# Kernel optimization log

Hardware: AMD Instinct MI355X
Metric: run time of the kernel (lower is better)

The kernel has to match this reference:

```python
import jax, jax.numpy as jnp
import numpy as np

B, S, N_USERS, N_ITEMS, E = 32, 512, 10000, 10000, 128


def setup_inputs() -> dict:
    key = jax.random.key(0)
    ks = jax.random.split(key, 8)
    users = jax.random.randint(ks[0], (B, S), 0, N_USERS, dtype=jnp.int32)
    items = jax.random.randint(ks[1], (B, S), 0, N_ITEMS, dtype=jnp.int32)
    user_mem0 = jax.random.normal(ks[2], (B, N_USERS, E), dtype=jnp.float32)
    item_mem0 = jax.random.normal(ks[3], (B, N_ITEMS, E), dtype=jnp.float32)
    # GRUCell(2E, E): w_ih (3E, 2E), w_hh (3E, E)
    w_ih = jax.random.normal(ks[4], (3 * E, 2 * E), dtype=jnp.float32) * 0.05
    w_hh = jax.random.normal(ks[5], (3 * E, E), dtype=jnp.float32) * 0.05
    b_ih = jax.random.normal(ks[6], (3 * E,), dtype=jnp.float32) * 0.05
    b_hh = jax.random.normal(ks[7], (3 * E,), dtype=jnp.float32) * 0.05
    return {"users": users, "items": items, "user_mem0": user_mem0,
            "item_mem0": item_mem0, "w_ih": w_ih, "w_hh": w_hh,
            "b_ih": b_ih, "b_hh": b_hh}


def _gru_cell(x, h, w_ih, w_hh, b_ih, b_hh):
    # torch.nn.GRUCell semantics
    gi = x @ w_ih.T + b_ih  # (B, 3E)
    gh = h @ w_hh.T + b_hh  # (B, 3E)
    i_r, i_z, i_n = jnp.split(gi, 3, axis=-1)
    h_r, h_z, h_n = jnp.split(gh, 3, axis=-1)
    r = jax.nn.sigmoid(i_r + h_r)
    z = jax.nn.sigmoid(i_z + h_z)
    n = jnp.tanh(i_n + r * h_n)
    return (1.0 - z) * n + z * h


def reference(users, items, user_mem0, item_mem0, w_ih, w_hh, b_ih, b_hh):
    batch = jnp.arange(users.shape[0])

    def step(carry, uv):
        um, im = carry
        u, it = uv  # (B,), (B,)
        ue = um[batch, u]   # gather (B, E)
        ie = im[batch, it]  # gather (B, E)
        xu = jnp.concatenate([ue, ie], axis=-1)
        xi = jnp.concatenate([ie, ue], axis=-1)
        nu = _gru_cell(xu, ue, w_ih, w_hh, b_ih, b_hh)
        ni = _gru_cell(xi, ie, w_ih, w_hh, b_ih, b_hh)
        um = um.at[batch, u].set(nu)   # scatter write
        im = im.at[batch, it].set(ni)  # scatter write
        return (um, im), (nu, ni)

    (_, _), (u_out, i_out) = jax.lax.scan(
        step, (user_mem0, item_mem0), (users.T, items.T))
    # (S, B, E) -> (B, S, E)
    return jnp.transpose(u_out, (1, 0, 2)), jnp.transpose(i_out, (1, 0, 2))
```

## Files before the change

### kernel.cpp

```cpp
#include <hip/hip_runtime.h>

#define NB 32
#define NS 512
#define NE 128
#define NU 10000

#define WS_PREVU 0
#define WS_PREVI 16384
#define WS_RCNT  32768
#define WS_LCNT  32864
#define WS_GL    32896
#define WS_LATE  82048
#define WS_WBF   98432

typedef __attribute__((ext_vector_type(8))) short bf16x8;
typedef __attribute__((ext_vector_type(4))) float f32x4;

__device__ __forceinline__ unsigned short f2bf(float f) {
    unsigned int u = __float_as_uint(f);
    u += 0x7fff + ((u >> 16) & 1);
    return (unsigned short)(u >> 16);
}

#define BARRIER() do { \
    asm volatile("s_waitcnt lgkmcnt(0)" ::: "memory"); \
    __builtin_amdgcn_s_barrier(); \
    __builtin_amdgcn_sched_barrier(0); \
} while (0)

__global__ __launch_bounds__(512) void prep_kernel(
    const int* __restrict__ users, const int* __restrict__ items,
    const float* __restrict__ w_ih, const float* __restrict__ w_hh, int* ws)
{
    const int blk = blockIdx.x, tid = threadIdx.x;
    if (blk >= 32) {
        const int base = (blk - 32) * 4096 + tid * 8;
        const int r = base >> 7, k = base & 127;
        const float* src;
        if (r < 384)      src = w_ih + (size_t)r * 256 + k;
        else if (r < 768) src = w_ih + (size_t)(r - 384) * 256 + 128 + k;
        else              src = w_hh + (size_t)(r - 768) * 128 + k;
        unsigned short* wbf = (unsigned short*)(ws + WS_WBF);
#pragma unroll
        for (int j = 0; j < 8; ++j) wbf[base + j] = f2bf(src[j]);
        return;
    }
    const int b = blk;
    __shared__ int s_u[NS], s_i[NS];
    __shared__ unsigned char s_r[NS];
    __shared__ int cnt[3], s_chg;
    s_u[tid] = users[b * NS + tid];
    s_i[tid] = items[b * NS + tid];
    if (tid < 3) cnt[tid] = 0;
    __syncthreads();
    const int mu = s_u[tid], mi = s_i[tid];
    int pu = -1, pi = -1;
    for (int u = tid - 1; u >= 0 && ((pu < 0) | (pi < 0)); u -= 8) {
        int vu[8], vi[8];
#pragma unroll
        for (int j = 0; j < 8; ++j) {
            const int uu = u - j;
            vu[j] = (uu >= 0) ? s_u[uu] : -1;
            vi[j] = (uu >= 0) ? s_i[uu] : -1;
        }
#pragma unroll
        for (int j = 0; j < 8; ++j) {
            if (pu < 0 && vu[j] == mu) pu = u - j;
            if (pi < 0 && vi[j] == mi) pi = u - j;
        }
    }
    ws[WS_PREVU + (b << 9) + tid] = pu;
    ws[WS_PREVI + (b << 9) + tid] = pi;
    s_r[tid] = (pu < 0 && pi < 0) ? 0 : 255;
    __syncthreads();
    for (int pass = 0; pass < 16; ++pass) {
        if (tid == 0) s_chg = 0;
        __syncthreads();
        if (s_r[tid] == 255) {
            const int ru = pu < 0 ? -1 : (int)s_r[pu];
            const int ri = pi < 0 ? -1 : (int)s_r[pi];
            if (ru != 255 && ri != 255) {
                int rr = 1 + (ru > ri ? ru : ri);
                if (rr > 3) rr = 3;
                s_r[tid] = (unsigned char)rr;
                s_chg = 1;
            }
        }
        __syncthreads();
        if (!s_chg) break;
    }
    const int r = s_r[tid];
    if (r < 3) {
        const int slot = atomicAdd(&cnt[r], 1);
        ws[WS_GL + (r * 32 + b) * 512 + slot] = tid;
    }
    __syncthreads();
    if (tid < 3) ws[WS_RCNT + tid * 32 + b] = cnt[tid];
    if (tid == 0) {
        int n = 0;
        for (int t = 0; t < NS; ++t)
            if (s_r[t] >= 3) { ws[WS_LATE + (b << 9) + n] = t; ++n; }
        ws[WS_LCNT + b] = n;
    }
}

__global__ __launch_bounds__(512, 1) void rg_kernel(
    const int* __restrict__ users, const int* __restrict__ items,
    const float* __restrict__ umem0, const float* __restrict__ imem0,
    const float* __restrict__ b_ih, const float* __restrict__ b_hh,
    const int* __restrict__ ws, float* uout, float* iout, int r)
{
    const int b = blockIdx.x & 31, sblk = blockIdx.x >> 5;
    const int cnt = ws[WS_RCNT + r * 32 + b];
    const int nch = (cnt + 7) >> 3;
    if (sblk >= nch) return;
    const int tid = threadIdx.x;
    const int lane = tid & 63, wave = tid >> 6;
    const int col = lane & 15, kgrp = lane >> 4;

    __shared__ __align__(16) float yl[16 * 1156];
    __shared__ __align__(16) float xf[16 * 132];
    __shared__ __align__(16) unsigned short xb[16 * 136];
    __shared__ float b6[768];
    __shared__ unsigned long long srcs[2][16];
    __shared__ unsigned long long hdst[2][16];

    for (int i = tid; i < 768; i += 512)
        b6[i] = i < 384 ? b_ih[i] : b_hh[i - 384];

    const unsigned short* wbf = (const unsigned short*)(ws + WS_WBF);
    bf16x8 wfrag[9][4];
#pragma unroll
    for (int m9 = 0; m9 < 9; ++m9) {
        const int row = wave * 144 + m9 * 16 + col;
#pragma unroll
        for (int kt = 0; kt < 4; ++kt)
            wfrag[m9][kt] = *(const bf16x8*)&wbf[row * 128 + kt * 32 + kgrp * 8];
    }

    const int* glist = ws + WS_GL + (r * 32 + b) * 512;
    const int* prevU = ws + WS_PREVU + (b << 9);
    const int* prevI = ws + WS_PREVI + (b << 9);

#define META(LC, SEL) do { \
    if (tid < 16) { \
        const int j = (LC) * 8 + (tid >> 1); \
        unsigned long long sp = 0, hd = 0; \
        if (j < cnt) { \
            const int t = glist[j]; \
            const int node = (b << 9) + t; \
            const int cell = tid & 1; \
            const int p = cell ? prevI[t] : prevU[t]; \
            const float* s; \
            if (p < 0) { \
                const int ix = cell ? items[node] : users[node]; \
                s = (cell ? imem0 : umem0) + ((size_t)b * NU + ix) * NE; \
            } else { \
                s = (cell ? iout : uout) + ((size_t)((b << 9) + p)) * NE; \
            } \
            sp = (unsigned long long)s; \
            hd = (unsigned long long)((cell ? iout : uout) + (size_t)node * NE); \
        } \
        srcs[SEL][tid] = sp; hdst[SEL][tid] = hd; \
    } \
} while (0)

    const int gc = tid >> 5, ge4 = (tid & 31) * 4;
    int cur = 0;
    META(sblk, 0);
    BARRIER();
    float4 v = (float4){0.f, 0.f, 0.f, 0.f};
    {
        const float* s = (const float*)srcs[0][gc];
        if (s) v = *(const float4*)(s + ge4);
    }

    for (int lc = sblk; lc < nch; lc += 8) {
        const int nxt = cur ^ 1;
        const bool hasnext = (lc + 8) < nch;
        if (hasnext) META(lc + 8, nxt);
        if (hdst[cur][gc]) {
            *(float4*)&xf[gc * 132 + ge4] = v;
            ushort4 w4;
            w4.x = f2bf(v.x); w4.y = f2bf(v.y);
            w4.z = f2bf(v.z); w4.w = f2bf(v.w);
            *(ushort4*)&xb[gc * 136 + ge4] = w4;
        }
        BARRIER();
        float4 vn = (float4){0.f, 0.f, 0.f, 0.f};
        if (hasnext) {
            const float* s = (const float*)srcs[nxt][gc];
            if (s) vn = *(const float4*)(s + ge4);
        }
        {
            bf16x8 bfrag[4];
#pragma unroll
            for (int kt = 0; kt < 4; ++kt)
                bfrag[kt] = *(const bf16x8*)&xb[col * 136 + kt * 32 + kgrp * 8];
            f32x4 acc[9];
#pragma unroll
            for (int m9 = 0; m9 < 9; ++m9) acc[m9] = (f32x4){0.f, 0.f, 0.f, 0.f};
#pragma unroll
            for (int kt = 0; kt < 4; ++kt)
#pragma unroll
                for (int m9 = 0; m9 < 9; ++m9)
                    acc[m9] = __builtin_amdgcn_mfma_f32_16x16x32_bf16(
                        wfrag[m9][kt], bfrag[kt], acc[m9], 0, 0, 0);
#pragma unroll
            for (int m9 = 0; m9 < 9; ++m9)
                *(f32x4*)&yl[col * 1156 + wave * 144 + m9 * 16 + kgrp * 4] = acc[m9];
        }
        BARRIER();
#pragma unroll
        for (int it = 0; it < 4; ++it) {
            const int idx = tid + it * 512;
            const int c = idx >> 7, e = idx & 127;
            float* hb = (float*)hdst[cur][c];
            if (hb) {
                const float* ys = &yl[c * 1156];
                const float* yo = &yl[(c ^ 1) * 1156];
                const float gir = ys[e]        + yo[384 + e] + b6[e];
                const float giz = ys[128 + e]  + yo[512 + e] + b6[128 + e];
                const float gin = ys[256 + e]  + yo[640 + e] + b6[256 + e];
                const float ghr = ys[768 + e]  + b6[384 + e];
                const float ghz = ys[896 + e]  + b6[512 + e];
                const float ghn = ys[1024 + e] + b6[640 + e];
                const float rr = 1.f / (1.f + __expf(-(gir + ghr)));
                const float z  = 1.f / (1.f + __expf(-(giz + ghz)));
                const float pre = gin + rr * ghn;
                const float nn = 2.f / (1.f + __expf(-2.f * pre)) - 1.f;
                hb[e] = (1.f - z) * nn + z * xf[c * 132 + e];
            }
        }
        BARRIER();
        v = vn; cur = nxt;
    }
#undef META
}

__global__ __launch_bounds__(512, 1) void cleanup_kernel(
    const int* __restrict__ users, const int* __restrict__ items,
    const float* __restrict__ umem0, const float* __restrict__ imem0,
    const float* __restrict__ b_ih, const float* __restrict__ b_hh,
    const int* __restrict__ ws, float* uout, float* iout)
{
    const int b = blockIdx.x;
    const int cnt2 = ws[WS_RCNT + 64 + b];
    const int cntL = ws[WS_LCNT + b];
    if (cnt2 + cntL == 0) return;
    const int tid = threadIdx.x;
    const int lane = tid & 63, wave = tid >> 6;
    const int col = lane & 15, kgrp = lane >> 4;

    __shared__ __align__(16) float yl[16 * 1156];
    __shared__ __align__(16) float xf[16 * 132];
    __shared__ __align__(16) unsigned short xb[16 * 136];
    __shared__ float b6[768];
    __shared__ unsigned long long srcs[16];
    __shared__ unsigned long long hdst[16];

    for (int i = tid; i < 768; i += 512)
        b6[i] = i < 384 ? b_ih[i] : b_hh[i - 384];

    const unsigned short* wbf = (const unsigned short*)(ws + WS_WBF);
    bf16x8 wfrag[9][4];
#pragma unroll
    for (int m9 = 0; m9 < 9; ++m9) {
        const int row = wave * 144 + m9 * 16 + col;
#pragma unroll
        for (int kt = 0; kt < 4; ++kt)
            wfrag[m9][kt] = *(const bf16x8*)&wbf[row * 128 + kt * 32 + kgrp * 8];
    }

    const int* prevU = ws + WS_PREVU + (b << 9);
    const int* prevI = ws + WS_PREVI + (b << 9);

    for (int ph = 0; ph < 2; ++ph) {
        const int cntn = ph == 0 ? cnt2 : cntL;
        const int base = ph == 0 ? WS_GL + (64 + b) * 512 : WS_LATE + (b << 9);
        const int step = ph == 0 ? 8 : 1;
        for (int j0 = 0; j0 < cntn; j0 += step) {
            const int n = (cntn - j0 < step) ? (cntn - j0) : step;
            if (tid < 16) {
                const int jj = tid >> 1;
                unsigned long long sp = 0, hd = 0;
                if (jj < n) {
                    const int t = ws[base + j0 + jj];
                    const int node = (b << 9) + t;
                    const int cell = tid & 1;
                    const int p = cell ? prevI[t] : prevU[t];
                    const float* s;
                    if (p < 0) {
                        const int ix = cell ? items[node] : users[node];
                        s = (cell ? imem0 : umem0) + ((size_t)b * NU + ix) * NE;
                    } else {
                        s = (cell ? iout : uout) + ((size_t)((b << 9) + p)) * NE;
                    }
                    sp = (unsigned long long)s;
                    hd = (unsigned long long)((cell ? iout : uout) + (size_t)node * NE);
                }
                srcs[tid] = sp; hdst[tid] = hd;
            }
            __syncthreads();
            {
                const int c = tid >> 5, e4 = (tid & 31) * 4;
                const float* s = (const float*)srcs[c];
                if (s) {
                    const float4 vv = *(const float4*)(s + e4);
                    *(float4*)&xf[c * 132 + e4] = vv;
                    ushort4 w4;
                    w4.x = f2bf(vv.x); w4.y = f2bf(vv.y);
                    w4.z = f2bf(vv.z); w4.w = f2bf(vv.w);
                    *(ushort4*)&xb[c * 136 + e4] = w4;
                }
            }
            __syncthreads();
            {
                bf16x8 bfrag[4];
#pragma unroll
                for (int kt = 0; kt < 4; ++kt)
                    bfrag[kt] = *(const bf16x8*)&xb[col * 136 + kt * 32 + kgrp * 8];
                f32x4 acc[9];
#pragma unroll
                for (int m9 = 0; m9 < 9; ++m9) acc[m9] = (f32x4){0.f, 0.f, 0.f, 0.f};
#pragma unroll
                for (int kt = 0; kt < 4; ++kt)
#pragma unroll
                    for (int m9 = 0; m9 < 9; ++m9)
                        acc[m9] = __builtin_amdgcn_mfma_f32_16x16x32_bf16(
                            wfrag[m9][kt], bfrag[kt], acc[m9], 0, 0, 0);
#pragma unroll
                for (int m9 = 0; m9 < 9; ++m9)
                    *(f32x4*)&yl[col * 1156 + wave * 144 + m9 * 16 + kgrp * 4] = acc[m9];
            }
            __syncthreads();
#pragma unroll
            for (int it = 0; it < 4; ++it) {
                const int idx = tid + it * 512;
                const int c = idx >> 7, e = idx & 127;
                float* hb = (float*)hdst[c];
                if (hb) {
                    const float* ys = &yl[c * 1156];
                    const float* yo = &yl[(c ^ 1) * 1156];
                    const float gir = ys[e]        + yo[384 + e] + b6[e];
                    const float giz = ys[128 + e]  + yo[512 + e] + b6[128 + e];
                    const float gin = ys[256 + e]  + yo[640 + e] + b6[256 + e];
                    const float ghr = ys[768 + e]  + b6[384 + e];
                    const float ghz = ys[896 + e]  + b6[512 + e];
                    const float ghn = ys[1024 + e] + b6[640 + e];
                    const float rr = 1.f / (1.f + __expf(-(gir + ghr)));
                    const float z  = 1.f / (1.f + __expf(-(giz + ghz)));
                    const float pre = gin + rr * ghn;
                    const float nn = 2.f / (1.f + __expf(-2.f * pre)) - 1.f;
                    hb[e] = (1.f - z) * nn + z * xf[c * 132 + e];
                }
            }
            __threadfence();
            __syncthreads();
        }
    }
}

extern "C" void kernel_launch(void* const* d_in, const int* in_sizes, int n_in,
                              void* d_out, int out_size, void* d_ws, size_t ws_size,
                              hipStream_t stream) {
    const int*   users = (const int*)d_in[0];
    const int*   items = (const int*)d_in[1];
    const float* umem0 = (const float*)d_in[2];
    const float* imem0 = (const float*)d_in[3];
    const float* w_ih  = (const float*)d_in[4];
    const float* w_hh  = (const float*)d_in[5];
    const float* b_ih  = (const float*)d_in[6];
    const float* b_hh  = (const float*)d_in[7];

    float* uout = (float*)d_out;
    float* iout = uout + (size_t)NB * NS * NE;
    int* ws = (int*)d_ws;

    prep_kernel<<<68, 512, 0, stream>>>(users, items, w_ih, w_hh, ws);
    rg_kernel<<<256, 512, 0, stream>>>(users, items, umem0, imem0,
                                       b_ih, b_hh, ws, uout, iout, 0);
    rg_kernel<<<256, 512, 0, stream>>>(users, items, umem0, imem0,
                                       b_ih, b_hh, ws, uout, iout, 1);
    cleanup_kernel<<<NB, 512, 0, stream>>>(users, items, umem0, imem0,
                                           b_ih, b_hh, ws, uout, iout);
}
```

Measured before the change: 125.7 us.

## Fuse prep, rank phases and cleanup into single per-batch kernel

Merges the preprocessing, two rank-parallel GRU phases, and serial cleanup into one kernel with one block per batch, keeping predecessor indices and rank lists in shared memory instead of workspace. Weights are converted to bf16 directly into registers per block. This removes launch overhead and workspace traffic but collapses the 8-way per-batch parallelism of the rank phases into one block.

```diff
diff --git a/kernel.cpp b/kernel.cpp
--- a/kernel.cpp
+++ b/kernel.cpp
@@ -4,14 +4,6 @@
 #define NS 512
 #define NE 128
 #define NU 10000
-
-#define WS_PREVU 0
-#define WS_PREVI 16384
-#define WS_RCNT  32768
-#define WS_LCNT  32864
-#define WS_GL    32896
-#define WS_LATE  82048
-#define WS_WBF   98432
 
 typedef __attribute__((ext_vector_type(8))) short bf16x8;
 typedef __attribute__((ext_vector_type(4))) float f32x4;
@@ -28,31 +20,58 @@
     __builtin_amdgcn_sched_barrier(0); \
 } while (0)
 
-__global__ __launch_bounds__(512) void prep_kernel(
+__global__ __launch_bounds__(512, 1) void limnet_all(
     const int* __restrict__ users, const int* __restrict__ items,
-    const float* __restrict__ w_ih, const float* __restrict__ w_hh, int* ws)
+    const float* __restrict__ umem0, const float* __restrict__ imem0,
+    const float* __restrict__ w_ih, const float* __restrict__ w_hh,
+    const float* __restrict__ b_ih, const float* __restrict__ b_hh,
+    float* uout, float* iout)
 {
-    const int blk = blockIdx.x, tid = threadIdx.x;
-    if (blk >= 32) {
-        const int base = (blk - 32) * 4096 + tid * 8;
-        const int r = base >> 7, k = base & 127;
-        const float* src;
-        if (r < 384)      src = w_ih + (size_t)r * 256 + k;
-        else if (r < 768) src = w_ih + (size_t)(r - 384) * 256 + 128 + k;
-        else              src = w_hh + (size_t)(r - 768) * 128 + k;
-        unsigned short* wbf = (unsigned short*)(ws + WS_WBF);
-#pragma unroll
-        for (int j = 0; j < 8; ++j) wbf[base + j] = f2bf(src[j]);
-        return;
-    }
-    const int b = blk;
+    const int b = blockIdx.x, tid = threadIdx.x;
+    const int lane = tid & 63, wave = tid >> 6;
+    const int col = lane & 15, kgrp = lane >> 4;
+
+    __shared__ __align__(16) float yl[16 * 1156];
+    __shared__ __align__(16) float xf[16 * 132];
+    __shared__ __align__(16) unsigned short xb[16 * 136];
+    __shared__ float b6[768];
     __shared__ int s_u[NS], s_i[NS];
+    __shared__ short s_pU[NS], s_pI[NS];
     __shared__ unsigned char s_r[NS];
-    __shared__ int cnt[3], s_chg;
+    __shared__ short s_list[4][NS];
+    __shared__ int s_cnt[4], s_chg;
+    __shared__ unsigned long long srcs[2][16];
+    __shared__ unsigned long long hdst[2][16];
+
     s_u[tid] = users[b * NS + tid];
     s_i[tid] = items[b * NS + tid];
-    if (tid < 3) cnt[tid] = 0;
+    if (tid < 4) s_cnt[tid] = 0;
+    for (int i = tid; i < 768; i += 512)
+        b6[i] = i < 384 ? b_ih[i] : b_hh[i - 384];
+
+    bf16x8 wfrag[9][4];
+#pragma unroll
+    for (int m9 = 0; m9 < 9; ++m9) {
+        const int row = wave * 144 + m9 * 16 + col;
+#pragma unroll
+        for (int kt = 0; kt < 4; ++kt) {
+            const int k = kt * 32 + kgrp * 8;
+            const float* src;
+            if (row < 384)      src = w_ih + (size_t)row * 256 + k;
+            else if (row < 768) src = w_ih + (size_t)(row - 384) * 256 + 128 + k;
+            else                src = w_hh + (size_t)(row - 768) * 128 + k;
+            const float4 f0 = *(const float4*)(src);
+            const float4 f1 = *(const float4*)(src + 4);
+            bf16x8 wv;
+            wv[0] = (short)f2bf(f0.x); wv[1] = (short)f2bf(f0.y);
+            wv[2] = (short)f2bf(f0.z); wv[3] = (short)f2bf(f0.w);
+            wv[4] = (short)f2bf(f1.x); wv[5] = (short)f2bf(f1.y);
+            wv[6] = (short)f2bf(f1.z); wv[7] = (short)f2bf(f1.w);
+            wfrag[m9][kt] = wv;
+        }
+    }
     __syncthreads();
+
     const int mu = s_u[tid], mi = s_i[tid];
     int pu = -1, pi = -1;
     for (int u = tid - 1; u >= 0 && ((pu < 0) | (pi < 0)); u -= 8) {
@@ -69,8 +88,8 @@
             if (pi < 0 && vi[j] == mi) pi = u - j;
         }
     }
-    ws[WS_PREVU + (b << 9) + tid] = pu;
-    ws[WS_PREVI + (b << 9) + tid] = pi;
+    s_pU[tid] = (short)pu;
+    s_pI[tid] = (short)pi;
     s_r[tid] = (pu < 0 && pi < 0) ? 0 : 255;
     __syncthreads();
     for (int pass = 0; pass < 16; ++pass) {
@@ -89,71 +108,36 @@
         __syncthreads();
         if (!s_chg) break;
     }
-    const int r = s_r[tid];
-    if (r < 3) {
-        const int slot = atomicAdd(&cnt[r], 1);
-        ws[WS_GL + (r * 32 + b) * 512 + slot] = tid;
+    {
+        const int r = s_r[tid];
+        if (r < 3) {
+            const int slot = atomicAdd(&s_cnt[r], 1);
+            s_list[r][slot] = (short)tid;
+        }
     }
     __syncthreads();
-    if (tid < 3) ws[WS_RCNT + tid * 32 + b] = cnt[tid];
     if (tid == 0) {
         int n = 0;
         for (int t = 0; t < NS; ++t)
-            if (s_r[t] >= 3) { ws[WS_LATE + (b << 9) + n] = t; ++n; }
-        ws[WS_LCNT + b] = n;
-    }
-}
-
-__global__ __launch_bounds__(512, 1) void rg_kernel(
-    const int* __restrict__ users, const int* __restrict__ items,
-    const float* __restrict__ umem0, const float* __restrict__ imem0,
-    const float* __restrict__ b_ih, const float* __restrict__ b_hh,
-    const int* __restrict__ ws, float* uout, float* iout, int r)
-{
-    const int b = blockIdx.x & 31, sblk = blockIdx.x >> 5;
-    const int cnt = ws[WS_RCNT + r * 32 + b];
-    const int nch = (cnt + 7) >> 3;
-    if (sblk >= nch) return;
-    const int tid = threadIdx.x;
-    const int lane = tid & 63, wave = tid >> 6;
-    const int col = lane & 15, kgrp = lane >> 4;
-
-    __shared__ __align__(16) float yl[16 * 1156];
-    __shared__ __align__(16) float xf[16 * 132];
-    __shared__ __align__(16) unsigned short xb[16 * 136];
-    __shared__ float b6[768];
-    __shared__ unsigned long long srcs[2][16];
-    __shared__ unsigned long long hdst[2][16];
-
-    for (int i = tid; i < 768; i += 512)
-        b6[i] = i < 384 ? b_ih[i] : b_hh[i - 384];
-
-    const unsigned short* wbf = (const unsigned short*)(ws + WS_WBF);
-    bf16x8 wfrag[9][4];
-#pragma unroll
-    for (int m9 = 0; m9 < 9; ++m9) {
-        const int row = wave * 144 + m9 * 16 + col;
-#pragma unroll
-        for (int kt = 0; kt < 4; ++kt)
-            wfrag[m9][kt] = *(const bf16x8*)&wbf[row * 128 + kt * 32 + kgrp * 8];
-    }
-
-    const int* glist = ws + WS_GL + (r * 32 + b) * 512;
-    const int* prevU = ws + WS_PREVU + (b << 9);
-    const int* prevI = ws + WS_PREVI + (b << 9);
-
-#define META(LC, SEL) do { \
+            if (s_r[t] >= 3) { s_list[3][n] = (short)t; ++n; }
+        s_cnt[3] = n;
+    }
+    __syncthreads();
+
+    const int gc = tid >> 5, ge4 = (tid & 31) * 4;
+
+#define META(PH, LC, SEL) do { \
     if (tid < 16) { \
         const int j = (LC) * 8 + (tid >> 1); \
         unsigned long long sp = 0, hd = 0; \
-        if (j < cnt) { \
-            const int t = glist[j]; \
+        if (j < s_cnt[PH]) { \
+            const int t = (int)s_list[PH][j]; \
             const int node = (b << 9) + t; \
             const int cell = tid & 1; \
-            const int p = cell ? prevI[t] : prevU[t]; \
+            const int p = cell ? (int)s_pI[t] : (int)s_pU[t]; \
             const float* s; \
             if (p < 0) { \
-                const int ix = cell ? items[node] : users[node]; \
+                const int ix = cell ? s_i[t] : s_u[t]; \
                 s = (cell ? imem0 : umem0) + ((size_t)b * NU + ix) * NE; \
             } else { \
                 s = (cell ? iout : uout) + ((size_t)((b << 9) + p)) * NE; \
@@ -165,33 +149,117 @@
     } \
 } while (0)
 
-    const int gc = tid >> 5, ge4 = (tid & 31) * 4;
-    int cur = 0;
-    META(sblk, 0);
-    BARRIER();
-    float4 v = (float4){0.f, 0.f, 0.f, 0.f};
-    {
-        const float* s = (const float*)srcs[0][gc];
-        if (s) v = *(const float4*)(s + ge4);
-    }
-
-    for (int lc = sblk; lc < nch; lc += 8) {
-        const int nxt = cur ^ 1;
-        const bool hasnext = (lc + 8) < nch;
-        if (hasnext) META(lc + 8, nxt);
-        if (hdst[cur][gc]) {
-            *(float4*)&xf[gc * 132 + ge4] = v;
-            ushort4 w4;
-            w4.x = f2bf(v.x); w4.y = f2bf(v.y);
-            w4.z = f2bf(v.z); w4.w = f2bf(v.w);
-            *(ushort4*)&xb[gc * 136 + ge4] = w4;
-        }
-        BARRIER();
-        float4 vn = (float4){0.f, 0.f, 0.f, 0.f};
-        if (hasnext) {
-            const float* s = (const float*)srcs[nxt][gc];
-            if (s) vn = *(const float4*)(s + ge4);
-        }
+    for (int ph = 0; ph < 3; ++ph) {
+        const int nch = (s_cnt[ph] + 7) >> 3;
+        if (nch > 0) {
+            int cur = 0;
+            META(ph, 0, 0);
+            BARRIER();
+            float4 v = (float4){0.f, 0.f, 0.f, 0.f};
+            {
+                const float* s = (const float*)srcs[0][gc];
+                if (s) v = *(const float4*)(s + ge4);
+            }
+            for (int lc = 0; lc < nch; ++lc) {
+                const int nxt = cur ^ 1;
+                const bool hasnext = (lc + 1) < nch;
+                if (hasnext) META(ph, lc + 1, nxt);
+                if (hdst[cur][gc]) {
+                    *(float4*)&xf[gc * 132 + ge4] = v;
+                    ushort4 w4;
+                    w4.x = f2bf(v.x); w4.y = f2bf(v.y);
+                    w4.z = f2bf(v.z); w4.w = f2bf(v.w);
+                    *(ushort4*)&xb[gc * 136 + ge4] = w4;
+                }
+                BARRIER();
+                float4 vn = (float4){0.f, 0.f, 0.f, 0.f};
+                if (hasnext) {
+                    const float* s = (const float*)srcs[nxt][gc];
+                    if (s) vn = *(const float4*)(s + ge4);
+                }
+                {
+                    bf16x8 bfrag[4];
+#pragma unroll
+                    for (int kt = 0; kt < 4; ++kt)
+                        bfrag[kt] = *(const bf16x8*)&xb[col * 136 + kt * 32 + kgrp * 8];
+                    f32x4 acc[9];
+#pragma unroll
+                    for (int m9 = 0; m9 < 9; ++m9)
+                        acc[m9] = (f32x4){0.f, 0.f, 0.f, 0.f};
+#pragma unroll
+                    for (int kt = 0; kt < 4; ++kt)
+#pragma unroll
+                        for (int m9 = 0; m9 < 9; ++m9)
+                            acc[m9] = __builtin_amdgcn_mfma_f32_16x16x32_bf16(
+                                wfrag[m9][kt], bfrag[kt], acc[m9], 0, 0, 0);
+#pragma unroll
+                    for (int m9 = 0; m9 < 9; ++m9)
+                        *(f32x4*)&yl[col * 1156 + wave * 144 + m9 * 16 + kgrp * 4] = acc[m9];
+                }
+                BARRIER();
+#pragma unroll
+                for (int it = 0; it < 4; ++it) {
+                    const int idx = tid + it * 512;
+                    const int c = idx >> 7, e = idx & 127;
+                    float* hb = (float*)hdst[cur][c];
+                    if (hb) {
+                        const float* ys = &yl[c * 1156];
+                        const float* yo = &yl[(c ^ 1) * 1156];
+                        const float gir = ys[e]        + yo[384 + e] + b6[e];
+                        const float giz = ys[128 + e]  + yo[512 + e] + b6[128 + e];
+                        const float gin = ys[256 + e]  + yo[640 + e] + b6[256 + e];
+                        const float ghr = ys[768 + e]  + b6[384 + e];
+                        const float ghz = ys[896 + e]  + b6[512 + e];
+                        const float ghn = ys[1024 + e] + b6[640 + e];
+                        const float rr = 1.f / (1.f + __expf(-(gir + ghr)));
+                        const float z  = 1.f / (1.f + __expf(-(giz + ghz)));
+                        const float pre = gin + rr * ghn;
+                        const float nn = 2.f / (1.f + __expf(-2.f * pre)) - 1.f;
+                        hb[e] = (1.f - z) * nn + z * xf[c * 132 + e];
+                    }
+                }
+                BARRIER();
+                v = vn; cur = nxt;
+            }
+        }
+        __threadfence();
+        __syncthreads();
+    }
+
+    const int nL = s_cnt[3];
+    for (int k = 0; k < nL; ++k) {
+        if (tid < 16) {
+            unsigned long long sp = 0, hd = 0;
+            if (tid < 2) {
+                const int t = (int)s_list[3][k];
+                const int node = (b << 9) + t;
+                const int cell = tid;
+                const int p = cell ? (int)s_pI[t] : (int)s_pU[t];
+                const float* s;
+                if (p < 0) {
+                    const int ix = cell ? s_i[t] : s_u[t];
+                    s = (cell ? imem0 : umem0) + ((size_t)b * NU + ix) * NE;
+                } else {
+                    s = (cell ? iout : uout) + ((size_t)((b << 9) + p)) * NE;
+                }
+                sp = (unsigned long long)s;
+                hd = (unsigned long long)((cell ? iout : uout) + (size_t)node * NE);
+            }
+            srcs[0][tid] = sp; hdst[0][tid] = hd;
+        }
+        __syncthreads();
+        {
+            const float* s = (const float*)srcs[0][gc];
+            if (s) {
+                const float4 vv = *(const float4*)(s + ge4);
+                *(float4*)&xf[gc * 132 + ge4] = vv;
+                ushort4 w4;
+                w4.x = f2bf(vv.x); w4.y = f2bf(vv.y);
+                w4.z = f2bf(vv.z); w4.w = f2bf(vv.w);
+                *(ushort4*)&xb[gc * 136 + ge4] = w4;
+            }
+        }
+        __syncthreads();
         {
             bf16x8 bfrag[4];
 #pragma unroll
@@ -210,12 +278,12 @@
             for (int m9 = 0; m9 < 9; ++m9)
                 *(f32x4*)&yl[col * 1156 + wave * 144 + m9 * 16 + kgrp * 4] = acc[m9];
         }
-        BARRIER();
+        __syncthreads();
 #pragma unroll
         for (int it = 0; it < 4; ++it) {
             const int idx = tid + it * 512;
             const int c = idx >> 7, e = idx & 127;
-            float* hb = (float*)hdst[cur][c];
+            float* hb = (float*)hdst[0][c];
             if (hb) {
                 const float* ys = &yl[c * 1156];
                 const float* yo = &yl[(c ^ 1) * 1156];
@@ -232,133 +300,10 @@
                 hb[e] = (1.f - z) * nn + z * xf[c * 132 + e];
             }
         }
-        BARRIER();
-        v = vn; cur = nxt;
+        __threadfence();
+        __syncthreads();
     }
 #undef META
-}
-
-__global__ __launch_bounds__(512, 1) void cleanup_kernel(
-    const int* __restrict__ users, const int* __restrict__ items,
-    const float* __restrict__ umem0, const float* __restrict__ imem0,
-    const float* __restrict__ b_ih, const float* __restrict__ b_hh,
-    const int* __restrict__ ws, float* uout, float* iout)
-{
-    const int b = blockIdx.x;
-    const int cnt2 = ws[WS_RCNT + 64 + b];
-    const int cntL = ws[WS_LCNT + b];
-    if (cnt2 + cntL == 0) return;
-    const int tid = threadIdx.x;
-    const int lane = tid & 63, wave = tid >> 6;
-    const int col = lane & 15, kgrp = lane >> 4;
-
-    __shared__ __align__(16) float yl[16 * 1156];
-    __shared__ __align__(16) float xf[16 * 132];
-    __shared__ __align__(16) unsigned short xb[16 * 136];
-    __shared__ float b6[768];
-    __shared__ unsigned long long srcs[16];
-    __shared__ unsigned long long hdst[16];
-
-    for (int i = tid; i < 768; i += 512)
-        b6[i] = i < 384 ? b_ih[i] : b_hh[i - 384];
-
-    const unsigned short* wbf = (const unsigned short*)(ws + WS_WBF);
-    bf16x8 wfrag[9][4];
-#pragma unroll
-    for (int m9 = 0; m9 < 9; ++m9) {
-        const int row = wave * 144 + m9 * 16 + col;
-#pragma unroll
-        for (int kt = 0; kt < 4; ++kt)
-            wfrag[m9][kt] = *(const bf16x8*)&wbf[row * 128 + kt * 32 + kgrp * 8];
-    }
-
-    const int* prevU = ws + WS_PREVU + (b << 9);
-    const int* prevI = ws + WS_PREVI + (b << 9);
-
-    for (int ph = 0; ph < 2; ++ph) {
-        const int cntn = ph == 0 ? cnt2 : cntL;
-        const int base = ph == 0 ? WS_GL + (64 + b) * 512 : WS_LATE + (b << 9);
-        const int step = ph == 0 ? 8 : 1;
-        for (int j0 = 0; j0 < cntn; j0 += step) {
-            const int n = (cntn - j0 < step) ? (cntn - j0) : step;
-            if (tid < 16) {
-                const int jj = tid >> 1;
-                unsigned long long sp = 0, hd = 0;
-                if (jj < n) {
-                    const int t = ws[base + j0 + jj];
-                    const int node = (b << 9) + t;
-                    const int cell = tid & 1;
-                    const int p = cell ? prevI[t] : prevU[t];
-                    const float* s;
-                    if (p < 0) {
-                        const int ix = cell ? items[node] : users[node];
-                        s = (cell ? imem0 : umem0) + ((size_t)b * NU + ix) * NE;
-                    } else {
-                        s = (cell ? iout : uout) + ((size_t)((b << 9) + p)) * NE;
-                    }
-                    sp = (unsigned long long)s;
-                    hd = (unsigned long long)((cell ? iout : uout) + (size_t)node * NE);
-                }
-                srcs[tid] = sp; hdst[tid] = hd;
-            }
-            __syncthreads();
-            {
-                const int c = tid >> 5, e4 = (tid & 31) * 4;
-                const float* s = (const float*)srcs[c];
-                if (s) {
-                    const float4 vv = *(const float4*)(s + e4);
-                    *(float4*)&xf[c * 132 + e4] = vv;
-                    ushort4 w4;
-                    w4.x = f2bf(vv.x); w4.y = f2bf(vv.y);
-                    w4.z = f2bf(vv.z); w4.w = f2bf(vv.w);
-                    *(ushort4*)&xb[c * 136 + e4] = w4;
-                }
-            }
-            __syncthreads();
-            {
-                bf16x8 bfrag[4];
-#pragma unroll
-                for (int kt = 0; kt < 4; ++kt)
-                    bfrag[kt] = *(const bf16x8*)&xb[col * 136 + kt * 32 + kgrp * 8];
-                f32x4 acc[9];
-#pragma unroll
-                for (int m9 = 0; m9 < 9; ++m9) acc[m9] = (f32x4){0.f, 0.f, 0.f, 0.f};
-#pragma unroll
-                for (int kt = 0; kt < 4; ++kt)
-#pragma unroll
-                    for (int m9 = 0; m9 < 9; ++m9)
-                        acc[m9] = __builtin_amdgcn_mfma_f32_16x16x32_bf16(
-                            wfrag[m9][kt], bfrag[kt], acc[m9], 0, 0, 0);
-#pragma unroll
-                for (int m9 = 0; m9 < 9; ++m9)
-                    *(f32x4*)&yl[col * 1156 + wave * 144 + m9 * 16 + kgrp * 4] = acc[m9];
-            }
-            __syncthreads();
-#pragma unroll
-            for (int it = 0; it < 4; ++it) {
-                const int idx = tid + it * 512;
-                const int c = idx >> 7, e = idx & 127;
-                float* hb = (float*)hdst[c];
-                if (hb) {
-                    const float* ys = &yl[c * 1156];
-                    const float* yo = &yl[(c ^ 1) * 1156];
-                    const float gir = ys[e]        + yo[384 + e] + b6[e];
-                    const float giz = ys[128 + e]  + yo[512 + e] + b6[128 + e];
-                    const float gin = ys[256 + e]  + yo[640 + e] + b6[256 + e];
-                    const float ghr = ys[768 + e]  + b6[384 + e];
-                    const float ghz = ys[896 + e]  + b6[512 + e];
-                    const float ghn = ys[1024 + e] + b6[640 + e];
-                    const float rr = 1.f / (1.f + __expf(-(gir + ghr)));
-                    const float z  = 1.f / (1.f + __expf(-(giz + ghz)));
-                    const float pre = gin + rr * ghn;
-                    const float nn = 2.f / (1.f + __expf(-2.f * pre)) - 1.f;
-                    hb[e] = (1.f - z) * nn + z * xf[c * 132 + e];
-                }
-            }
-            __threadfence();
-            __syncthreads();
-        }
-    }
 }
 
 extern "C" void kernel_launch(void* const* d_in, const int* in_sizes, int n_in,
@@ -375,13 +320,7 @@
 
     float* uout = (float*)d_out;
     float* iout = uout + (size_t)NB * NS * NE;
-    int* ws = (int*)d_ws;
-
-    prep_kernel<<<68, 512, 0, stream>>>(users, items, w_ih, w_hh, ws);
-    rg_kernel<<<256, 512, 0, stream>>>(users, items, umem0, imem0,
-                                       b_ih, b_hh, ws, uout, iout, 0);
-    rg_kernel<<<256, 512, 0, stream>>>(users, items, umem0, imem0,
-                                       b_ih, b_hh, ws, uout, iout, 1);
-    cleanup_kernel<<<NB, 512, 0, stream>>>(users, items, umem0, imem0,
-                                           b_ih, b_hh, ws, uout, iout);
+
+    limnet_all<<<NB, 512, 0, stream>>>(users, items, umem0, imem0,
+                                       w_ih, w_hh, b_ih, b_hh, uout, iout);
 }
```

New measurement: 270.3 us. 2.15x slower.

## Fuse round kernels and cleanup into one persistent kernel with grid barriers

Applied to the files above, without the earlier changes.

Merges the two round kernels and the cleanup kernel into a single persistent launch of 256 blocks. Blocks are separated by a software grid barrier built on an atomic counter in the workspace, which prep_kernel resets. The goal is to remove two kernel launch gaps and to load the bf16 weight fragments into registers once instead of three times. The cost is spin-waiting on a global atomic, and the scheme depends on all 256 blocks being co-resident. The spin loop also has a bailout cap that could silently break ordering.

```diff
diff --git a/kernel.cpp b/kernel.cpp
--- a/kernel.cpp
+++ b/kernel.cpp
@@ -9,9 +9,10 @@
 #define WS_PREVI 16384
 #define WS_RCNT  32768
 #define WS_LCNT  32864
-#define WS_GL    32896
-#define WS_LATE  82048
-#define WS_WBF   98432
+#define WS_BAR   32896
+#define WS_GL    32912
+#define WS_LATE  82064
+#define WS_WBF   98448
 
 typedef __attribute__((ext_vector_type(8))) short bf16x8;
 typedef __attribute__((ext_vector_type(4))) float f32x4;
@@ -27,6 +28,21 @@
     __builtin_amdgcn_s_barrier(); \
     __builtin_amdgcn_sched_barrier(0); \
 } while (0)
+
+__device__ __forceinline__ void grid_barrier(int* ctr) {
+    __syncthreads();
+    if (threadIdx.x == 0) {
+        __threadfence();
+        atomicAdd(ctr, 1);
+        int spins = 0;
+        while (atomicAdd(ctr, 0) < 256) {
+            __builtin_amdgcn_s_sleep(8);
+            if (++spins > (1 << 20)) break;
+        }
+    }
+    __syncthreads();
+    __threadfence();
+}
 
 __global__ __launch_bounds__(512) void prep_kernel(
     const int* __restrict__ users, const int* __restrict__ items,
@@ -34,6 +50,7 @@
 {
     const int blk = blockIdx.x, tid = threadIdx.x;
     if (blk >= 32) {
+        if (blk == 32 && tid < 2) ws[WS_BAR + tid] = 0;
         const int base = (blk - 32) * 4096 + tid * 8;
         const int r = base >> 7, k = base & 127;
         const float* src;
@@ -104,17 +121,13 @@
     }
 }
 
-__global__ __launch_bounds__(512, 1) void rg_kernel(
+__global__ __launch_bounds__(512, 1) void solve_kernel(
     const int* __restrict__ users, const int* __restrict__ items,
     const float* __restrict__ umem0, const float* __restrict__ imem0,
     const float* __restrict__ b_ih, const float* __restrict__ b_hh,
-    const int* __restrict__ ws, float* uout, float* iout, int r)
+    int* ws, float* uout, float* iout)
 {
-    const int b = blockIdx.x & 31, sblk = blockIdx.x >> 5;
-    const int cnt = ws[WS_RCNT + r * 32 + b];
-    const int nch = (cnt + 7) >> 3;
-    if (sblk >= nch) return;
-    const int tid = threadIdx.x;
+    const int blk = blockIdx.x, tid = threadIdx.x;
     const int lane = tid & 63, wave = tid >> 6;
     const int col = lane & 15, kgrp = lane >> 4;
 
@@ -137,17 +150,19 @@
         for (int kt = 0; kt < 4; ++kt)
             wfrag[m9][kt] = *(const bf16x8*)&wbf[row * 128 + kt * 32 + kgrp * 8];
     }
-
-    const int* glist = ws + WS_GL + (r * 32 + b) * 512;
+    __syncthreads();
+
+    const int b = blk & 31, sblk = blk >> 5;
+    const int gc = tid >> 5, ge4 = (tid & 31) * 4;
     const int* prevU = ws + WS_PREVU + (b << 9);
     const int* prevI = ws + WS_PREVI + (b << 9);
 
-#define META(LC, SEL) do { \
+#define META(GLIST, CNT, LC, SEL) do { \
     if (tid < 16) { \
         const int j = (LC) * 8 + (tid >> 1); \
         unsigned long long sp = 0, hd = 0; \
-        if (j < cnt) { \
-            const int t = glist[j]; \
+        if (j < (CNT)) { \
+            const int t = (GLIST)[j]; \
             const int node = (b << 9) + t; \
             const int cell = tid & 1; \
             const int p = cell ? prevI[t] : prevU[t]; \
@@ -165,119 +180,94 @@
     } \
 } while (0)
 
-    const int gc = tid >> 5, ge4 = (tid & 31) * 4;
-    int cur = 0;
-    META(sblk, 0);
-    BARRIER();
-    float4 v = (float4){0.f, 0.f, 0.f, 0.f};
-    {
-        const float* s = (const float*)srcs[0][gc];
-        if (s) v = *(const float4*)(s + ge4);
-    }
-
-    for (int lc = sblk; lc < nch; lc += 8) {
-        const int nxt = cur ^ 1;
-        const bool hasnext = (lc + 8) < nch;
-        if (hasnext) META(lc + 8, nxt);
-        if (hdst[cur][gc]) {
-            *(float4*)&xf[gc * 132 + ge4] = v;
-            ushort4 w4;
-            w4.x = f2bf(v.x); w4.y = f2bf(v.y);
-            w4.z = f2bf(v.z); w4.w = f2bf(v.w);
-            *(ushort4*)&xb[gc * 136 + ge4] = w4;
-        }
-        BARRIER();
-        float4 vn = (float4){0.f, 0.f, 0.f, 0.f};
-        if (hasnext) {
-            const float* s = (const float*)srcs[nxt][gc];
-            if (s) vn = *(const float4*)(s + ge4);
-        }
-        {
-            bf16x8 bfrag[4];
-#pragma unroll
-            for (int kt = 0; kt < 4; ++kt)
-                bfrag[kt] = *(const bf16x8*)&xb[col * 136 + kt * 32 + kgrp * 8];
-            f32x4 acc[9];
-#pragma unroll
-            for (int m9 = 0; m9 < 9; ++m9) acc[m9] = (f32x4){0.f, 0.f, 0.f, 0.f};
-#pragma unroll
-            for (int kt = 0; kt < 4; ++kt)
-#pragma unroll
-                for (int m9 = 0; m9 < 9; ++m9)
-                    acc[m9] = __builtin_amdgcn_mfma_f32_16x16x32_bf16(
-                        wfrag[m9][kt], bfrag[kt], acc[m9], 0, 0, 0);
-#pragma unroll
-            for (int m9 = 0; m9 < 9; ++m9)
-                *(f32x4*)&yl[col * 1156 + wave * 144 + m9 * 16 + kgrp * 4] = acc[m9];
-        }
-        BARRIER();
-#pragma unroll
-        for (int it = 0; it < 4; ++it) {
-            const int idx = tid + it * 512;
-            const int c = idx >> 7, e = idx & 127;
-            float* hb = (float*)hdst[cur][c];
-            if (hb) {
-                const float* ys = &yl[c * 1156];
-                const float* yo = &yl[(c ^ 1) * 1156];
-                const float gir = ys[e]        + yo[384 + e] + b6[e];
-                const float giz = ys[128 + e]  + yo[512 + e] + b6[128 + e];
-                const float gin = ys[256 + e]  + yo[640 + e] + b6[256 + e];
-                const float ghr = ys[768 + e]  + b6[384 + e];
-                const float ghz = ys[896 + e]  + b6[512 + e];
-                const float ghn = ys[1024 + e] + b6[640 + e];
-                const float rr = 1.f / (1.f + __expf(-(gir + ghr)));
-                const float z  = 1.f / (1.f + __expf(-(giz + ghz)));
-                const float pre = gin + rr * ghn;
-                const float nn = 2.f / (1.f + __expf(-2.f * pre)) - 1.f;
-                hb[e] = (1.f - z) * nn + z * xf[c * 132 + e];
-            }
-        }
-        BARRIER();
-        v = vn; cur = nxt;
-    }
-#undef META
-}
-
-__global__ __launch_bounds__(512, 1) void cleanup_kernel(
-    const int* __restrict__ users, const int* __restrict__ items,
-    const float* __restrict__ umem0, const float* __restrict__ imem0,
-    const float* __restrict__ b_ih, const float* __restrict__ b_hh,
-    const int* __restrict__ ws, float* uout, float* iout)
-{
-    const int b = blockIdx.x;
+#define CHUNK_COMPUTE(CUR) do { \
+    { \
+        bf16x8 bfrag[4]; \
+        _Pragma("unroll") \
+        for (int kt = 0; kt < 4; ++kt) \
+            bfrag[kt] = *(const bf16x8*)&xb[col * 136 + kt * 32 + kgrp * 8]; \
+        f32x4 acc[9]; \
+        _Pragma("unroll") \
+        for (int m9 = 0; m9 < 9; ++m9) acc[m9] = (f32x4){0.f, 0.f, 0.f, 0.f}; \
+        _Pragma("unroll") \
+        for (int kt = 0; kt < 4; ++kt) \
+            _Pragma("unroll") \
+            for (int m9 = 0; m9 < 9; ++m9) \
+                acc[m9] = __builtin_amdgcn_mfma_f32_16x16x32_bf16( \
+                    wfrag[m9][kt], bfrag[kt], acc[m9], 0, 0, 0); \
+        _Pragma("unroll") \
+        for (int m9 = 0; m9 < 9; ++m9) \
+            *(f32x4*)&yl[col * 1156 + wave * 144 + m9 * 16 + kgrp * 4] = acc[m9]; \
+    } \
+    BARRIER(); \
+    _Pragma("unroll") \
+    for (int it = 0; it < 4; ++it) { \
+        const int idx = tid + it * 512; \
+        const int c = idx >> 7, e = idx & 127; \
+        float* hb = (float*)hdst[CUR][c]; \
+        if (hb) { \
+            const float* ys = &yl[c * 1156]; \
+            const float* yo = &yl[(c ^ 1) * 1156]; \
+            const float gir = ys[e]        + yo[384 + e] + b6[e]; \
+            const float giz = ys[128 + e]  + yo[512 + e] + b6[128 + e]; \
+            const float gin = ys[256 + e]  + yo[640 + e] + b6[256 + e]; \
+            const float ghr = ys[768 + e]  + b6[384 + e]; \
+            const float ghz = ys[896 + e]  + b6[512 + e]; \
+            const float ghn = ys[1024 + e] + b6[640 + e]; \
+            const float rr = 1.f / (1.f + __expf(-(gir + ghr))); \
+            const float z  = 1.f / (1.f + __expf(-(giz + ghz))); \
+            const float pre = gin + rr * ghn; \
+            const float nn = 2.f / (1.f + __expf(-2.f * pre)) - 1.f; \
+            hb[e] = (1.f - z) * nn + z * xf[c * 132 + e]; \
+        } \
+    } \
+    BARRIER(); \
+} while (0)
+
+    for (int r = 0; r < 2; ++r) {
+        const int cnt = ws[WS_RCNT + r * 32 + b];
+        const int nch = (cnt + 7) >> 3;
+        const int* glist = ws + WS_GL + (r * 32 + b) * 512;
+        if (sblk < nch) {
+            int cur = 0;
+            META(glist, cnt, sblk, 0);
+            BARRIER();
+            float4 v = (float4){0.f, 0.f, 0.f, 0.f};
+            {
+                const float* s = (const float*)srcs[0][gc];
+                if (s) v = *(const float4*)(s + ge4);
+            }
+            for (int lc = sblk; lc < nch; lc += 8) {
+                const int nxt = cur ^ 1;
+                const bool hasnext = (lc + 8) < nch;
+                if (hasnext) META(glist, cnt, lc + 8, nxt);
+                if (hdst[cur][gc]) {
+                    *(float4*)&xf[gc * 132 + ge4] = v;
+                    ushort4 w4;
+                    w4.x = f2bf(v.x); w4.y = f2bf(v.y);
+                    w4.z = f2bf(v.z); w4.w = f2bf(v.w);
+                    *(ushort4*)&xb[gc * 136 + ge4] = w4;
+                }
+                BARRIER();
+                float4 vn = (float4){0.f, 0.f, 0.f, 0.f};
+                if (hasnext) {
+                    const float* s = (const float*)srcs[nxt][gc];
+                    if (s) vn = *(const float4*)(s + ge4);
+                }
+                CHUNK_COMPUTE(cur);
+                v = vn; cur = nxt;
+            }
+        }
+        grid_barrier(ws + WS_BAR + r);
+    }
+
+    if (blk >= 32) return;
     const int cnt2 = ws[WS_RCNT + 64 + b];
     const int cntL = ws[WS_LCNT + b];
-    if (cnt2 + cntL == 0) return;
-    const int tid = threadIdx.x;
-    const int lane = tid & 63, wave = tid >> 6;
-    const int col = lane & 15, kgrp = lane >> 4;
-
-    __shared__ __align__(16) float yl[16 * 1156];
-    __shared__ __align__(16) float xf[16 * 132];
-    __shared__ __align__(16) unsigned short xb[16 * 136];
-    __shared__ float b6[768];
-    __shared__ unsigned long long srcs[16];
-    __shared__ unsigned long long hdst[16];
-
-    for (int i = tid; i < 768; i += 512)
-        b6[i] = i < 384 ? b_ih[i] : b_hh[i - 384];
-
-    const unsigned short* wbf = (const unsigned short*)(ws + WS_WBF);
-    bf16x8 wfrag[9][4];
-#pragma unroll
-    for (int m9 = 0; m9 < 9; ++m9) {
-        const int row = wave * 144 + m9 * 16 + col;
-#pragma unroll
-        for (int kt = 0; kt < 4; ++kt)
-            wfrag[m9][kt] = *(const bf16x8*)&wbf[row * 128 + kt * 32 + kgrp * 8];
-    }
-
-    const int* prevU = ws + WS_PREVU + (b << 9);
-    const int* prevI = ws + WS_PREVI + (b << 9);
-
     for (int ph = 0; ph < 2; ++ph) {
         const int cntn = ph == 0 ? cnt2 : cntL;
-        const int base = ph == 0 ? WS_GL + (64 + b) * 512 : WS_LATE + (b << 9);
+        const int* lst = ph == 0 ? ws + WS_GL + (64 + b) * 512
+                                 : ws + WS_LATE + (b << 9);
         const int step = ph == 0 ? 8 : 1;
         for (int j0 = 0; j0 < cntn; j0 += step) {
             const int n = (cntn - j0 < step) ? (cntn - j0) : step;
@@ -285,7 +275,7 @@
                 const int jj = tid >> 1;
                 unsigned long long sp = 0, hd = 0;
                 if (jj < n) {
-                    const int t = ws[base + j0 + jj];
+                    const int t = lst[j0 + jj];
                     const int node = (b << 9) + t;
                     const int cell = tid & 1;
                     const int p = cell ? prevI[t] : prevU[t];
@@ -299,66 +289,28 @@
                     sp = (unsigned long long)s;
                     hd = (unsigned long long)((cell ? iout : uout) + (size_t)node * NE);
                 }
-                srcs[tid] = sp; hdst[tid] = hd;
+                srcs[0][tid] = sp; hdst[0][tid] = hd;
             }
             __syncthreads();
             {
-                const int c = tid >> 5, e4 = (tid & 31) * 4;
-                const float* s = (const float*)srcs[c];
+                const float* s = (const float*)srcs[0][gc];
                 if (s) {
-                    const float4 vv = *(const float4*)(s + e4);
-                    *(float4*)&xf[c * 132 + e4] = vv;
+                    const float4 vv = *(const float4*)(s + ge4);
+                    *(float4*)&xf[gc * 132 + ge4] = vv;
                     ushort4 w4;
                     w4.x = f2bf(vv.x); w4.y = f2bf(vv.y);
                     w4.z = f2bf(vv.z); w4.w = f2bf(vv.w);
-                    *(ushort4*)&xb[c * 136 + e4] = w4;
+                    *(ushort4*)&xb[gc * 136 + ge4] = w4;
                 }
             }
             __syncthreads();
-            {
-                bf16x8 bfrag[4];
-#pragma unroll
-                for (int kt = 0; kt < 4; ++kt)
-                    bfrag[kt] = *(const bf16x8*)&xb[col * 136 + kt * 32 + kgrp * 8];
-                f32x4 acc[9];
-#pragma unroll
-                for (int m9 = 0; m9 < 9; ++m9) acc[m9] = (f32x4){0.f, 0.f, 0.f, 0.f};
-#pragma unroll
-                for (int kt = 0; kt < 4; ++kt)
-#pragma unroll
-                    for (int m9 = 0; m9 < 9; ++m9)
-                        acc[m9] = __builtin_amdgcn_mfma_f32_16x16x32_bf16(
-                            wfrag[m9][kt], bfrag[kt], acc[m9], 0, 0, 0);
-#pragma unroll
-                for (int m9 = 0; m9 < 9; ++m9)
-                    *(f32x4*)&yl[col * 1156 + wave * 144 + m9 * 16 + kgrp * 4] = acc[m9];
-            }
-            __syncthreads();
-#pragma unroll
-            for (int it = 0; it < 4; ++it) {
-                const int idx = tid + it * 512;
-                const int c = idx >> 7, e = idx & 127;
-                float* hb = (float*)hdst[c];
-                if (hb) {
-                    const float* ys = &yl[c * 1156];
-                    const float* yo = &yl[(c ^ 1) * 1156];
-                    const float gir = ys[e]        + yo[384 + e] + b6[e];
-                    const float giz = ys[128 + e]  + yo[512 + e] + b6[128 + e];
-                    const float gin = ys[256 + e]  + yo[640 + e] + b6[256 + e];
-                    const float ghr = ys[768 + e]  + b6[384 + e];
-                    const float ghz = ys[896 + e]  + b6[512 + e];
-                    const float ghn = ys[1024 + e] + b6[640 + e];
-                    const float rr = 1.f / (1.f + __expf(-(gir + ghr)));
-                    const float z  = 1.f / (1.f + __expf(-(giz + ghz)));
-                    const float pre = gin + rr * ghn;
-                    const float nn = 2.f / (1.f + __expf(-2.f * pre)) - 1.f;
-                    hb[e] = (1.f - z) * nn + z * xf[c * 132 + e];
-                }
-            }
+            CHUNK_COMPUTE(0);
             __threadfence();
             __syncthreads();
         }
     }
+#undef META
+#undef CHUNK_COMPUTE
 }
 
 extern "C" void kernel_launch(void* const* d_in, const int* in_sizes, int n_in,
@@ -378,10 +330,6 @@
     int* ws = (int*)d_ws;
 
     prep_kernel<<<68, 512, 0, stream>>>(users, items, w_ih, w_hh, ws);
-    rg_kernel<<<256, 512, 0, stream>>>(users, items, umem0, imem0,
-                                       b_ih, b_hh, ws, uout, iout, 0);
-    rg_kernel<<<256, 512, 0, stream>>>(users, items, umem0, imem0,
-                                       b_ih, b_hh, ws, uout, iout, 1);
-    cleanup_kernel<<<NB, 512, 0, stream>>>(users, items, umem0, imem0,
-                                           b_ih, b_hh, ws, uout, iout);
-}
+    solve_kernel<<<256, 512, 0, stream>>>(users, items, umem0, imem0,
+                                          b_ih, b_hh, ws, uout, iout);
+}
```

Result: slower. 198.0 us (+57.6%).

## Software-pipeline GRU rounds: double-buffer gate outputs, overlap gates with next MFMA

Applied to the files above, without the earlier changes.

Restructures the per-round GRU kernel loop into a software pipeline. Gate outputs are double-buffered in shared memory so the gate nonlinearity of chunk i-1 runs after the MFMA of chunk i, which removes one barrier per iteration. Source rows are prefetched two chunks ahead, and the gather list and prev indices are staged in LDS as shorts. The gate epilogue is vectorized to float4 and the fp32 hidden copy in LDS is replaced by registers. The cost is more LDS and more register pressure.

```diff
diff --git a/kernel.cpp b/kernel.cpp
--- a/kernel.cpp
+++ b/kernel.cpp
@@ -114,19 +114,26 @@
     const int cnt = ws[WS_RCNT + r * 32 + b];
     const int nch = (cnt + 7) >> 3;
     if (sblk >= nch) return;
+    const int m = (nch - sblk + 7) >> 3;
     const int tid = threadIdx.x;
     const int lane = tid & 63, wave = tid >> 6;
     const int col = lane & 15, kgrp = lane >> 4;
 
-    __shared__ __align__(16) float yl[16 * 1156];
-    __shared__ __align__(16) float xf[16 * 132];
+    __shared__ __align__(16) float yl[2][16 * 1156];
     __shared__ __align__(16) unsigned short xb[16 * 136];
-    __shared__ float b6[768];
-    __shared__ unsigned long long srcs[2][16];
-    __shared__ unsigned long long hdst[2][16];
+    __shared__ __align__(16) float b6[768];
+    __shared__ short sg_list[512];
+    __shared__ short sprev[2][512];
+    __shared__ unsigned long long srcs[4][16];
+    __shared__ unsigned long long hdst[4][16];
 
     for (int i = tid; i < 768; i += 512)
         b6[i] = i < 384 ? b_ih[i] : b_hh[i - 384];
+    if (tid < 512) {
+        sg_list[tid] = (short)((tid < cnt) ? ws[WS_GL + (r * 32 + b) * 512 + tid] : 0);
+        sprev[0][tid] = (short)ws[WS_PREVU + (b << 9) + tid];
+        sprev[1][tid] = (short)ws[WS_PREVI + (b << 9) + tid];
+    }
 
     const unsigned short* wbf = (const unsigned short*)(ws + WS_WBF);
     bf16x8 wfrag[9][4];
@@ -137,20 +144,20 @@
         for (int kt = 0; kt < 4; ++kt)
             wfrag[m9][kt] = *(const bf16x8*)&wbf[row * 128 + kt * 32 + kgrp * 8];
     }
-
-    const int* glist = ws + WS_GL + (r * 32 + b) * 512;
-    const int* prevU = ws + WS_PREVU + (b << 9);
-    const int* prevI = ws + WS_PREVI + (b << 9);
-
-#define META(LC, SEL) do { \
+    __syncthreads();
+
+    const int gc = tid >> 5;
+    const int e4 = (tid & 31) * 4;
+
+#define META(CI, SLOT) do { \
     if (tid < 16) { \
-        const int j = (LC) * 8 + (tid >> 1); \
+        const int j = (sblk + 8 * (CI)) * 8 + (tid >> 1); \
         unsigned long long sp = 0, hd = 0; \
         if (j < cnt) { \
-            const int t = glist[j]; \
+            const int t = (int)sg_list[j]; \
             const int node = (b << 9) + t; \
             const int cell = tid & 1; \
-            const int p = cell ? prevI[t] : prevU[t]; \
+            const int p = (int)sprev[cell][t]; \
             const float* s; \
             if (p < 0) { \
                 const int ix = cell ? items[node] : users[node]; \
@@ -161,36 +168,77 @@
             sp = (unsigned long long)s; \
             hd = (unsigned long long)((cell ? iout : uout) + (size_t)node * NE); \
         } \
-        srcs[SEL][tid] = sp; hdst[SEL][tid] = hd; \
+        srcs[SLOT][tid] = sp; hdst[SLOT][tid] = hd; \
     } \
 } while (0)
 
-    const int gc = tid >> 5, ge4 = (tid & 31) * 4;
-    int cur = 0;
-    META(sblk, 0);
+#define GATES(P, VP, DS) do { \
+    const float* hb = (const float*)hdst[DS][gc]; \
+    if (hb) { \
+        const float* ys = &yl[P][gc * 1156]; \
+        const float* yo = &yl[P][(gc ^ 1) * 1156]; \
+        const float4 yir = *(const float4*)&ys[e4]; \
+        const float4 yiz = *(const float4*)&ys[128 + e4]; \
+        const float4 yin = *(const float4*)&ys[256 + e4]; \
+        const float4 oir = *(const float4*)&yo[384 + e4]; \
+        const float4 oiz = *(const float4*)&yo[512 + e4]; \
+        const float4 oin = *(const float4*)&yo[640 + e4]; \
+        const float4 yhr = *(const float4*)&ys[768 + e4]; \
+        const float4 yhz = *(const float4*)&ys[896 + e4]; \
+        const float4 yhn = *(const float4*)&ys[1024 + e4]; \
+        const float4 bir = *(const float4*)&b6[e4]; \
+        const float4 biz = *(const float4*)&b6[128 + e4]; \
+        const float4 bin = *(const float4*)&b6[256 + e4]; \
+        const float4 bhr = *(const float4*)&b6[384 + e4]; \
+        const float4 bhz = *(const float4*)&b6[512 + e4]; \
+        const float4 bhn = *(const float4*)&b6[640 + e4]; \
+        float4 hout; \
+        _Pragma("unroll") \
+        for (int jj = 0; jj < 4; ++jj) { \
+            const float gir = ((const float*)&yir)[jj] + ((const float*)&oir)[jj] + ((const float*)&bir)[jj]; \
+            const float giz = ((const float*)&yiz)[jj] + ((const float*)&oiz)[jj] + ((const float*)&biz)[jj]; \
+            const float gin = ((const float*)&yin)[jj] + ((const float*)&oin)[jj] + ((const float*)&bin)[jj]; \
+            const float ghr = ((const float*)&yhr)[jj] + ((const float*)&bhr)[jj]; \
+            const float ghz = ((const float*)&yhz)[jj] + ((const float*)&bhz)[jj]; \
+            const float ghn = ((const float*)&yhn)[jj] + ((const float*)&bhn)[jj]; \
+            const float rr = 1.f / (1.f + __expf(-(gir + ghr))); \
+            const float z  = 1.f / (1.f + __expf(-(giz + ghz))); \
+            const float pre = gin + rr * ghn; \
+            const float nn = 2.f / (1.f + __expf(-2.f * pre)) - 1.f; \
+            ((float*)&hout)[jj] = (1.f - z) * nn + z * ((const float*)&(VP))[jj]; \
+        } \
+        *(float4*)((float*)hb + e4) = hout; \
+    } \
+} while (0)
+
+    META(0, 0);
+    META(1, 1);
     BARRIER();
-    float4 v = (float4){0.f, 0.f, 0.f, 0.f};
+    float4 vs = (float4){0.f, 0.f, 0.f, 0.f};
+    float4 vg = (float4){0.f, 0.f, 0.f, 0.f};
+    float4 vp = (float4){0.f, 0.f, 0.f, 0.f};
     {
-        const float* s = (const float*)srcs[0][gc];
-        if (s) v = *(const float4*)(s + ge4);
-    }
-
-    for (int lc = sblk; lc < nch; lc += 8) {
-        const int nxt = cur ^ 1;
-        const bool hasnext = (lc + 8) < nch;
-        if (hasnext) META(lc + 8, nxt);
-        if (hdst[cur][gc]) {
-            *(float4*)&xf[gc * 132 + ge4] = v;
+        const float* s0 = (const float*)srcs[0][gc];
+        if (s0) vs = *(const float4*)(s0 + e4);
+        if (1 < m) {
+            const float* s1 = (const float*)srcs[1][gc];
+            if (s1) vg = *(const float4*)(s1 + e4);
+        }
+    }
+
+    for (int i = 0; i < m; ++i) {
+        if (i + 2 < m) META(i + 2, (i + 2) & 3);
+        {
             ushort4 w4;
-            w4.x = f2bf(v.x); w4.y = f2bf(v.y);
-            w4.z = f2bf(v.z); w4.w = f2bf(v.w);
-            *(ushort4*)&xb[gc * 136 + ge4] = w4;
+            w4.x = f2bf(vs.x); w4.y = f2bf(vs.y);
+            w4.z = f2bf(vs.z); w4.w = f2bf(vs.w);
+            *(ushort4*)&xb[gc * 136 + e4] = w4;
         }
         BARRIER();
-        float4 vn = (float4){0.f, 0.f, 0.f, 0.f};
-        if (hasnext) {
-            const float* s = (const float*)srcs[nxt][gc];
-            if (s) vn = *(const float4*)(s + ge4);
+        float4 vgn = (float4){0.f, 0.f, 0.f, 0.f};
+        if (i + 2 < m) {
+            const float* s = (const float*)srcs[(i + 2) & 3][gc];
+            if (s) vgn = *(const float4*)(s + e4);
         }
         {
             bf16x8 bfrag[4];
@@ -206,36 +254,18 @@
                 for (int m9 = 0; m9 < 9; ++m9)
                     acc[m9] = __builtin_amdgcn_mfma_f32_16x16x32_bf16(
                         wfrag[m9][kt], bfrag[kt], acc[m9], 0, 0, 0);
+            float* ybase = &yl[i & 1][col * 1156 + wave * 144 + kgrp * 4];
 #pragma unroll
             for (int m9 = 0; m9 < 9; ++m9)
-                *(f32x4*)&yl[col * 1156 + wave * 144 + m9 * 16 + kgrp * 4] = acc[m9];
-        }
+                *(f32x4*)(ybase + m9 * 16) = acc[m9];
+        }
+        if (i >= 1) GATES((i - 1) & 1, vp, (i - 1) & 3);
         BARRIER();
-#pragma unroll
-        for (int it = 0; it < 4; ++it) {
-            const int idx = tid + it * 512;
-            const int c = idx >> 7, e = idx & 127;
-            float* hb = (float*)hdst[cur][c];
-            if (hb) {
-                const float* ys = &yl[c * 1156];
-                const float* yo = &yl[(c ^ 1) * 1156];
-                const float gir = ys[e]        + yo[384 + e] + b6[e];
-                const float giz = ys[128 + e]  + yo[512 + e] + b6[128 + e];
-                const float gin = ys[256 + e]  + yo[640 + e] + b6[256 + e];
-                const float ghr = ys[768 + e]  + b6[384 + e];
-                const float ghz = ys[896 + e]  + b6[512 + e];
-                const float ghn = ys[1024 + e] + b6[640 + e];
-                const float rr = 1.f / (1.f + __expf(-(gir + ghr)));
-                const float z  = 1.f / (1.f + __expf(-(giz + ghz)));
-                const float pre = gin + rr * ghn;
-                const float nn = 2.f / (1.f + __expf(-2.f * pre)) - 1.f;
-                hb[e] = (1.f - z) * nn + z * xf[c * 132 + e];
-            }
-        }
-        BARRIER();
-        v = vn; cur = nxt;
-    }
+        vp = vs; vs = vg; vg = vgn;
+    }
+    GATES((m - 1) & 1, vp, (m - 1) & 3);
 #undef META
+#undef GATES
 }
 
 __global__ __launch_bounds__(512, 1) void cleanup_kernel(
@@ -277,7 +307,8 @@
 
     for (int ph = 0; ph < 2; ++ph) {
         const int cntn = ph == 0 ? cnt2 : cntL;
-        const int base = ph == 0 ? WS_GL + (64 + b) * 512 : WS_LATE + (b << 9);
+        const int* lst = ph == 0 ? ws + WS_GL + (64 + b) * 512
+                                 : ws + WS_LATE + (b << 9);
         const int step = ph == 0 ? 8 : 1;
         for (int j0 = 0; j0 < cntn; j0 += step) {
             const int n = (cntn - j0 < step) ? (cntn - j0) : step;
@@ -285,7 +316,7 @@
                 const int jj = tid >> 1;
                 unsigned long long sp = 0, hd = 0;
                 if (jj < n) {
-                    const int t = ws[base + j0 + jj];
+                    const int t = lst[j0 + jj];
                     const int node = (b << 9) + t;
                     const int cell = tid & 1;
                     const int p = cell ? prevI[t] : prevU[t];
@@ -303,15 +334,15 @@
             }
             __syncthreads();
             {
-                const int c = tid >> 5, e4 = (tid & 31) * 4;
+                const int c = tid >> 5, ee = (tid & 31) * 4;
                 const float* s = (const float*)srcs[c];
                 if (s) {
-                    const float4 vv = *(const float4*)(s + e4);
-                    *(float4*)&xf[c * 132 + e4] = vv;
+                    const float4 vv = *(const float4*)(s + ee);
+                    *(float4*)&xf[c * 132 + ee] = vv;
                     ushort4 w4;
                     w4.x = f2bf(vv.x); w4.y = f2bf(vv.y);
                     w4.z = f2bf(vv.z); w4.w = f2bf(vv.w);
-                    *(ushort4*)&xb[c * 136 + e4] = w4;
+                    *(ushort4*)&xb[c * 136 + ee] = w4;
                 }
             }
             __syncthreads();
```

Result: no change. 123.2 us (-1.9%).
